# Optimization experiments

Measured on AMD Instinct MI355X. Metric: run time of the kernel, lower is better.

Reference implementation:

```python
import jax, jax.numpy as jnp
import numpy as np

B, L, E, H = 4, 2048, 512, 8
HD = E // H
EPS = 1e-6


def setup_inputs() -> dict:
    key = jax.random.key(0)
    ks = jax.random.split(key, 9)
    s = 0.02
    return {
        "query": jax.random.normal(ks[0], (B, L, E), dtype=jnp.float32),
        "Wq": jax.random.normal(ks[1], (E, E), dtype=jnp.float32) * s,
        "bq": jnp.zeros((E,), dtype=jnp.float32),
        "Wk": jax.random.normal(ks[2], (E, E), dtype=jnp.float32) * s,
        "bk": jnp.zeros((E,), dtype=jnp.float32),
        "Wv": jax.random.normal(ks[3], (E, E), dtype=jnp.float32) * s,
        "bv": jnp.zeros((E,), dtype=jnp.float32),
        "Wo": jax.random.normal(ks[4], (E, E), dtype=jnp.float32) * s,
        "bo": jnp.zeros((E,), dtype=jnp.float32),
    }


def reference(query, Wq, bq, Wk, bk, Wv, bv, Wo, bo):
    b, tgt_len, embed_dim = query.shape
    n_head = H
    head_dim = embed_dim // n_head
    # Faithful to the source: a raw view (reshape), NOT a transpose.
    x = query.reshape(tgt_len, b, embed_dim)  # (L, B, E)
    q = x @ Wq.T + bq
    k = x @ Wk.T + bk
    v = x @ Wv.T + bv
    # softmax over head_dim, per head
    q = jax.nn.softmax(q.reshape(tgt_len, b, n_head, head_dim), axis=-1)
    k = jax.nn.softmax(k.reshape(tgt_len, b, n_head, head_dim), axis=-1)
    # (L, B*H, hd) -> (B*H, L, hd)
    q_ = q.reshape(tgt_len, b * n_head, head_dim).swapaxes(0, 1)
    k_ = k.reshape(tgt_len, b * n_head, head_dim).swapaxes(0, 1)
    comp_q_ = 1.0 - q_
    comp_k_ = 1.0 - k_
    v_ = v.reshape(tgt_len, b * n_head, head_dim).swapaxes(0, 1)
    # non-causal XNor attention: scores from q.k^T + (1-q).(1-k)^T
    weights = jnp.einsum('nld,nsd->nls', q_, k_) + jnp.einsum('nld,nsd->nls', comp_q_, comp_k_)
    denom = jnp.clip(jnp.sum(weights, axis=-1, keepdims=True), EPS, None)
    attn_weights = weights / denom
    attn_output = jnp.einsum('nls,nsd->nld', attn_weights, v_)  # (B*H, L, hd)
    attn_output = attn_output.swapaxes(0, 1).reshape(tgt_len, b, embed_dim)
    out = attn_output @ Wo.T + bo
    return out.reshape(b, tgt_len, embed_dim)
```

## Files before the change

kernel.cpp:

```cpp
#include <hip/hip_runtime.h>

#define B_ 4
#define L_ 2048
#define E_ 512
#define H_ 8
#define NROW (B_*L_)
#define SZ (NROW*E_)
#define NH (B_*H_)

typedef unsigned short u16;
typedef unsigned int u32;
typedef __attribute__((ext_vector_type(8))) __bf16 bf16x8;
typedef __attribute__((ext_vector_type(8))) u16 u16x8;
typedef __attribute__((ext_vector_type(4))) float f32x4;

__device__ __forceinline__ u16 f2bf(float f) {
  union { float f; u32 u; } v; v.f = f;
  u32 r = v.u + 0x7FFFu + ((v.u >> 16) & 1u);
  return (u16)(r >> 16);
}
__device__ __forceinline__ float bf2f(u16 s) {
  union { u32 u; float f; } v; v.u = ((u32)s) << 16;
  return v.f;
}
__device__ __forceinline__ void async16(const u16* g, u16* l) {
  __builtin_amdgcn_global_load_lds(
      (const __attribute__((address_space(1))) u32*)g,
      (__attribute__((address_space(3))) u32*)l, 16, 0, 0);
}

__global__ __launch_bounds__(256) void cvt_all(const float* __restrict__ X,
    const float* __restrict__ W0, const float* __restrict__ W1,
    const float* __restrict__ W2, const float* __restrict__ W3,
    u16* __restrict__ Y, u16* __restrict__ Y0, u16* __restrict__ Y1,
    u16* __restrict__ Y2, u16* __restrict__ Y3) {
  const int bid = blockIdx.x;
  const float* src;
  u16* dst;
  int off;
  if (bid < 2048) { src = X; dst = Y; off = bid * 2048; }
  else {
    const int t = bid - 2048, s = t >> 7, r = t & 127;
    src = (s == 0) ? W0 : (s == 1) ? W1 : (s == 2) ? W2 : W3;
    dst = (s == 0) ? Y0 : (s == 1) ? Y1 : (s == 2) ? Y2 : Y3;
    off = r * 2048;
  }
  const int i0 = off + threadIdx.x * 8;
  f32x4 a = *(const f32x4*)(src + i0);
  f32x4 b = *(const f32x4*)(src + i0 + 4);
  u16x8 o;
#pragma unroll
  for (int j = 0; j < 4; ++j) { o[j] = f2bf(a[j]); o[4 + j] = f2bf(b[j]); }
  *(u16x8*)(dst + i0) = o;
}

__global__ __launch_bounds__(256) void qkv_gemm(const u16* __restrict__ X,
    const u16* __restrict__ Wq, const u16* __restrict__ Wk, const u16* __restrict__ Wv,
    const float* __restrict__ bq, const float* __restrict__ bk, const float* __restrict__ bv,
    u16* __restrict__ Qo, u16* __restrict__ Ko, u16* __restrict__ Vo) {
  __shared__ __align__(16) union {
    struct { u16 a[2][128 * 32]; u16 b[2][64 * 32]; } st;
    u16 ep[4][16 * 72];
  } sh;
  const int z = blockIdx.z;
  const u16* W = (z == 0) ? Wq : (z == 1) ? Wk : Wv;
  const float* bias = (z == 0) ? bq : (z == 1) ? bk : bv;
  u16* C = (z == 0) ? Qo : (z == 1) ? Ko : Vo;
  const int tid = threadIdx.x;
  const int w = tid >> 6, lane = tid & 63;
  const int bm = blockIdx.x * 128, bn = blockIdx.y * 64;
  const int fr = lane & 15, quad = lane >> 4;
  const int c0 = tid, c1 = tid + 256;
  const int ar0 = c0 >> 2, ak0 = (c0 & 3) * 8;
  const int ar1 = c1 >> 2, ak1 = (c1 & 3) * 8;
  f32x4 acc[2][4] = {};
  for (int k0 = 0; k0 < E_; k0 += 64) {
    __syncthreads();
#pragma unroll
    for (int p = 0; p < 2; ++p) {
      const int kp = k0 + p * 32;
      async16(X + (size_t)(bm + ar0) * E_ + kp + ak0, sh.st.a[p] + c0 * 8);
      async16(X + (size_t)(bm + ar1) * E_ + kp + ak1, sh.st.a[p] + c1 * 8);
      async16(W + (size_t)(bn + ar0) * E_ + kp + ak0, sh.st.b[p] + c0 * 8);
    }
    __syncthreads();
#pragma unroll
    for (int p = 0; p < 2; ++p) {
      bf16x8 af[2], bf[4];
#pragma unroll
      for (int mt = 0; mt < 2; ++mt)
        af[mt] = *(const bf16x8*)(sh.st.a[p] + (w * 32 + mt * 16 + fr) * 32 + quad * 8);
#pragma unroll
      for (int nt = 0; nt < 4; ++nt)
        bf[nt] = *(const bf16x8*)(sh.st.b[p] + (nt * 16 + fr) * 32 + quad * 8);
#pragma unroll
      for (int mt = 0; mt < 2; ++mt)
#pragma unroll
        for (int nt = 0; nt < 4; ++nt)
          acc[mt][nt] = __builtin_amdgcn_mfma_f32_16x16x32_bf16(af[mt], bf[nt],
                                                                acc[mt][nt], 0, 0, 0);
    }
  }
  __syncthreads();
  u16* ep = sh.ep[w];
#pragma unroll
  for (int mt = 0; mt < 2; ++mt) {
    if (z < 2) {
#pragma unroll
      for (int r = 0; r < 4; ++r) {
        float v[4];
#pragma unroll
        for (int nt = 0; nt < 4; ++nt)
          v[nt] = acc[mt][nt][r] + bias[bn + nt * 16 + fr];
        float mx = fmaxf(fmaxf(v[0], v[1]), fmaxf(v[2], v[3]));
#pragma unroll
        for (int off = 1; off < 16; off <<= 1) mx = fmaxf(mx, __shfl_xor(mx, off, 64));
        float e[4], ssum = 0.f;
#pragma unroll
        for (int nt = 0; nt < 4; ++nt) { e[nt] = __expf(v[nt] - mx); ssum += e[nt]; }
#pragma unroll
        for (int off = 1; off < 16; off <<= 1) ssum += __shfl_xor(ssum, off, 64);
        const float inv = 1.f / ssum;
#pragma unroll
        for (int nt = 0; nt < 4; ++nt)
          ep[(quad * 4 + r) * 72 + nt * 16 + fr] = f2bf(e[nt] * inv);
      }
    } else {
#pragma unroll
      for (int r = 0; r < 4; ++r)
#pragma unroll
        for (int nt = 0; nt < 4; ++nt)
          ep[(quad * 4 + r) * 72 + nt * 16 + fr] = f2bf(acc[mt][nt][r] + bias[bn + nt * 16 + fr]);
    }
#pragma unroll
    for (int pass = 0; pass < 2; ++pass) {
      const int row = pass * 8 + (lane >> 3), ch = lane & 7;
      u16x8 val = *(const u16x8*)(ep + row * 72 + ch * 8);
      *(u16x8*)(C + (size_t)(bm + w * 32 + mt * 16 + row) * E_ + bn + ch * 8) = val;
    }
  }
}

__global__ __launch_bounds__(256) void gemm_out(const u16* __restrict__ X,
    const u16* __restrict__ W, const float* __restrict__ bias, float* __restrict__ C) {
  __shared__ __align__(16) union {
    struct { u16 a[2][128 * 32]; u16 b[2][64 * 32]; } st;
    float ep[4][16 * 68];
  } sh;
  const int tid = threadIdx.x;
  const int w = tid >> 6, lane = tid & 63;
  const int bm = blockIdx.x * 128, bn = blockIdx.y * 64;
  const int fr = lane & 15, quad = lane >> 4;
  const int c0 = tid, c1 = tid + 256;
  const int ar0 = c0 >> 2, ak0 = (c0 & 3) * 8;
  const int ar1 = c1 >> 2, ak1 = (c1 & 3) * 8;
  f32x4 acc[2][4] = {};
  for (int k0 = 0; k0 < E_; k0 += 64) {
    __syncthreads();
#pragma unroll
    for (int p = 0; p < 2; ++p) {
      const int kp = k0 + p * 32;
      async16(X + (size_t)(bm + ar0) * E_ + kp + ak0, sh.st.a[p] + c0 * 8);
      async16(X + (size_t)(bm + ar1) * E_ + kp + ak1, sh.st.a[p] + c1 * 8);
      async16(W + (size_t)(bn + ar0) * E_ + kp + ak0, sh.st.b[p] + c0 * 8);
    }
    __syncthreads();
#pragma unroll
    for (int p = 0; p < 2; ++p) {
      bf16x8 af[2], bf[4];
#pragma unroll
      for (int mt = 0; mt < 2; ++mt)
        af[mt] = *(const bf16x8*)(sh.st.a[p] + (w * 32 + mt * 16 + fr) * 32 + quad * 8);
#pragma unroll
      for (int nt = 0; nt < 4; ++nt)
        bf[nt] = *(const bf16x8*)(sh.st.b[p] + (nt * 16 + fr) * 32 + quad * 8);
#pragma unroll
      for (int mt = 0; mt < 2; ++mt)
#pragma unroll
        for (int nt = 0; nt < 4; ++nt)
          acc[mt][nt] = __builtin_amdgcn_mfma_f32_16x16x32_bf16(af[mt], bf[nt],
                                                                acc[mt][nt], 0, 0, 0);
    }
  }
  __syncthreads();
  float* ep = sh.ep[w];
#pragma unroll
  for (int mt = 0; mt < 2; ++mt) {
#pragma unroll
    for (int r = 0; r < 4; ++r)
#pragma unroll
      for (int nt = 0; nt < 4; ++nt)
        ep[(quad * 4 + r) * 68 + nt * 16 + fr] = acc[mt][nt][r] + bias[bn + nt * 16 + fr];
#pragma unroll
    for (int p = 0; p < 4; ++p) {
      const int id = p * 64 + lane;
      const int row = id >> 4, ch = id & 15;
      f32x4 val = *(const f32x4*)(ep + row * 68 + ch * 4);
      *(f32x4*)(C + (size_t)(bm + w * 32 + mt * 16 + row) * E_ + bn + ch * 4) = val;
    }
  }
}

__global__ __launch_bounds__(256) void kv_part(const u16* __restrict__ K,
    const u16* __restrict__ V, float* __restrict__ Part,
    float* __restrict__ KPart, float* __restrict__ VPart) {
  const int n = blockIdx.x, b = n >> 3, h = n & 7;
  const int sy = blockIdx.y;
  const int tid = threadIdx.x;
  const int td = tid & 15, te = tid >> 4;
  __shared__ float sK[32][68], sV[32][68];
  float acc[4][4] = {};
  float srow = 0.f;
  const int which = tid >> 7, sub = tid & 127;
  const int lr = sub >> 2, ck = (sub & 3) * 16;
  const u16* src = which ? V : K;
  float* dstrow = which ? &sV[lr][ck] : &sK[lr][ck];
  const int l0beg = sy * 128;
  for (int l0 = l0beg; l0 < l0beg + 128; l0 += 32) {
    const u16* g = src + (size_t)((l0 + lr) * B_ + b) * E_ + h * 64 + ck;
    u16x8 d0 = *(const u16x8*)g;
    u16x8 d1 = *(const u16x8*)(g + 8);
    __syncthreads();
    f32x4 f0, f1, f2, f3;
#pragma unroll
    for (int j = 0; j < 4; ++j) {
      f0[j] = bf2f(d0[j]); f1[j] = bf2f(d0[4 + j]);
      f2[j] = bf2f(d1[j]); f3[j] = bf2f(d1[4 + j]);
    }
    *(f32x4*)(dstrow) = f0; *(f32x4*)(dstrow + 4) = f1;
    *(f32x4*)(dstrow + 8) = f2; *(f32x4*)(dstrow + 12) = f3;
    __syncthreads();
#pragma unroll 8
    for (int p = 0; p < 32; ++p) {
      f32x4 kk = *(const f32x4*)&sK[p][td * 4];
      f32x4 vv = *(const f32x4*)&sV[p][te * 4];
#pragma unroll
      for (int i = 0; i < 4; ++i)
#pragma unroll
        for (int j = 0; j < 4; ++j)
          acc[i][j] = fmaf(kk[i], vv[j], acc[i][j]);
      if (tid < 64) srow += sK[p][tid];
      else if (tid < 128) srow += sV[p][tid - 64];
    }
  }
  float* Pp = Part + (size_t)(n * 16 + sy) * 4096;
#pragma unroll
  for (int j = 0; j < 4; ++j) {
    f32x4 v4 = {acc[0][j], acc[1][j], acc[2][j], acc[3][j]};
    *(f32x4*)(Pp + (te * 4 + j) * 64 + td * 4) = v4;
  }
  if (tid < 64) KPart[(n * 16 + sy) * 64 + tid] = srow;
  else if (tid < 128) VPart[(n * 16 + sy) * 64 + tid - 64] = srow;
}

__global__ __launch_bounds__(256) void kv_merge(const float* __restrict__ Part,
    const float* __restrict__ KPart, const float* __restrict__ VPart,
    float* __restrict__ Mt, float* __restrict__ Ks, float* __restrict__ Vs) {
  const int bid = blockIdx.x, tid = threadIdx.x;
  if (bid < 512) {
    const int oi = bid * 256 + tid;
    const int n = oi >> 12, j = oi & 4095;
    const float* p = Part + (size_t)n * 16 * 4096 + j;
    float s = 0.f;
#pragma unroll
    for (int sl = 0; sl < 16; ++sl) s += p[sl * 4096];
    Mt[oi] = s;
  } else {
    const int i = (bid - 512) * 256 + tid;
    const int which = i >> 11, rem = i & 2047;
    const int n = rem >> 6, d = rem & 63;
    const float* p = (which ? VPart : KPart) + (n * 16) * 64 + d;
    float s = 0.f;
#pragma unroll
    for (int sl = 0; sl < 16; ++sl) s += p[sl * 64];
    if (which) Vs[n * 64 + d] = s; else Ks[n * 64 + d] = s;
  }
}

__global__ __launch_bounds__(256) void apply_mfma(const u16* __restrict__ Qbf,
    const float* __restrict__ Mt, const float* __restrict__ Ksum,
    const float* __restrict__ Vsum, u16* __restrict__ Abf) {
  __shared__ __align__(16) u16 sQ[128 * 64];
  __shared__ __align__(16) u16 sM[64 * 64];
  __shared__ float sKs[64], sVs[64], sDen[128];
  const int n = blockIdx.x, b = n >> 3, h = n & 7;
  const int l0 = blockIdx.y * 128;
  const int tid = threadIdx.x, w = tid >> 6, lane = tid & 63;
  const int fr = lane & 15, quad = lane >> 4;
#pragma unroll
  for (int j = 0; j < 4; ++j) {
    const int rloc = w * 32 + j * 8;
    const int row = rloc + (lane >> 3);
    const int k = (lane & 7) * 8;
    async16(Qbf + (size_t)((l0 + row) * B_ + b) * E_ + h * 64 + k, sQ + rloc * 64);
  }
  {
    const float* Mp = Mt + (size_t)n * 4096 + tid * 16;
    f32x4 m0 = *(const f32x4*)(Mp);
    f32x4 m1 = *(const f32x4*)(Mp + 4);
    f32x4 m2 = *(const f32x4*)(Mp + 8);
    f32x4 m3 = *(const f32x4*)(Mp + 12);
    u16x8 o0, o1;
#pragma unroll
    for (int j = 0; j < 4; ++j) {
      o0[j] = f2bf(m0[j]); o0[4 + j] = f2bf(m1[j]);
      o1[j] = f2bf(m2[j]); o1[4 + j] = f2bf(m3[j]);
    }
    *(u16x8*)(sM + tid * 16) = o0;
    *(u16x8*)(sM + tid * 16 + 8) = o1;
  }
  if (tid < 64) sKs[tid] = Ksum[n * 64 + tid];
  else if (tid < 128) sVs[tid - 64] = Vsum[n * 64 + tid - 64];
  __syncthreads();
  union { u16x8 u; bf16x8 bv; } aU[2][2];
  bf16x8 bF[4][2];
#pragma unroll
  for (int mt = 0; mt < 2; ++mt)
#pragma unroll
    for (int ks = 0; ks < 2; ++ks)
      aU[mt][ks].u = *(const u16x8*)(sQ + (w * 32 + mt * 16 + fr) * 64 + ks * 32 + quad * 8);
#pragma unroll
  for (int nt = 0; nt < 4; ++nt)
#pragma unroll
    for (int ks = 0; ks < 2; ++ks)
      bF[nt][ks] = *(const bf16x8*)(sM + (nt * 16 + fr) * 64 + ks * 32 + quad * 8);
  float pden[2] = {0.f, 0.f};
#pragma unroll
  for (int mt = 0; mt < 2; ++mt)
#pragma unroll
    for (int ks = 0; ks < 2; ++ks)
#pragma unroll
      for (int j = 0; j < 8; ++j)
        pden[mt] = fmaf(bf2f(aU[mt][ks].u[j]), sKs[ks * 32 + quad * 8 + j], pden[mt]);
#pragma unroll
  for (int mt = 0; mt < 2; ++mt) {
    pden[mt] += __shfl_xor(pden[mt], 16, 64);
    pden[mt] += __shfl_xor(pden[mt], 32, 64);
    if (quad == 0)
      sDen[w * 32 + mt * 16 + fr] = fmaxf(2.f * pden[mt] + 62.f * (float)L_, 1e-6f);
  }
  __syncthreads();
  f32x4 acc[2][4];
#pragma unroll
  for (int mt = 0; mt < 2; ++mt)
#pragma unroll
    for (int nt = 0; nt < 4; ++nt) {
      const float iv = 31.f * sVs[nt * 16 + fr];
      acc[mt][nt] = (f32x4){iv, iv, iv, iv};
#pragma unroll
      for (int ks = 0; ks < 2; ++ks)
        acc[mt][nt] = __builtin_amdgcn_mfma_f32_16x16x32_bf16(aU[mt][ks].bv, bF[nt][ks],
                                                              acc[mt][nt], 0, 0, 0);
    }
#pragma unroll
  for (int mt = 0; mt < 2; ++mt)
#pragma unroll
    for (int r = 0; r < 4; ++r) {
      const int rloc = w * 32 + mt * 16 + quad * 4 + r;
      const float invd = 2.f / sDen[rloc];
      const size_t orow = (size_t)((l0 + rloc) * B_ + b) * E_ + h * 64;
#pragma unroll
      for (int nt = 0; nt < 4; ++nt)
        Abf[orow + nt * 16 + fr] = f2bf(acc[mt][nt][r] * invd);
    }
}

extern "C" void kernel_launch(void* const* d_in, const int* in_sizes, int n_in,
                              void* d_out, int out_size, void* d_ws, size_t ws_size,
                              hipStream_t stream) {
  const float* query = (const float*)d_in[0];
  const float* Wq = (const float*)d_in[1];
  const float* bq = (const float*)d_in[2];
  const float* Wk = (const float*)d_in[3];
  const float* bk = (const float*)d_in[4];
  const float* Wv = (const float*)d_in[5];
  const float* bv = (const float*)d_in[6];
  const float* Wo = (const float*)d_in[7];
  const float* bo = (const float*)d_in[8];
  float* out = (float*)d_out;

  char* ws = (char*)d_ws;
  u16* Xbf  = (u16*)(ws);
  u16* Qbf  = (u16*)(ws + 8388608);
  u16* Kbf  = (u16*)(ws + 16777216);
  u16* Vbf  = (u16*)(ws + 25165824);
  u16* Abf  = (u16*)(ws + 33554432);
  u16* Wqb  = (u16*)(ws + 41943040);
  u16* Wkb  = (u16*)(ws + 42467328);
  u16* Wvb  = (u16*)(ws + 42991616);
  u16* Wob  = (u16*)(ws + 43515904);
  float* Mt = (float*)(ws + 44040192);
  float* Ks = (float*)(ws + 44564480);
  float* Vs = (float*)(ws + 44572672);
  float* KPart = (float*)(ws + 44580864);
  float* VPart = (float*)(ws + 44711936);
  float* Part  = (float*)Xbf;

  cvt_all<<<2560, 256, 0, stream>>>(query, Wq, Wk, Wv, Wo,
                                    Xbf, Wqb, Wkb, Wvb, Wob);
  qkv_gemm<<<dim3(NROW / 128, E_ / 64, 3), 256, 0, stream>>>(
      Xbf, Wqb, Wkb, Wvb, bq, bk, bv, Qbf, Kbf, Vbf);
  kv_part<<<dim3(NH, 16), 256, 0, stream>>>(Kbf, Vbf, Part, KPart, VPart);
  kv_merge<<<528, 256, 0, stream>>>(Part, KPart, VPart, Mt, Ks, Vs);
  apply_mfma<<<dim3(NH, L_ / 128), 256, 0, stream>>>(Qbf, Mt, Ks, Vs, Abf);
  gemm_out<<<dim3(NROW / 128, E_ / 64), 256, 0, stream>>>(Abf, Wob, bo, out);
}
```

Measured before the change: 145.6 us.

## Widen QKV GEMM tile to 128x128 and store merged KV state as bf16

The QKV projection GEMM now uses 128x128 output tiles, with each of the four waves computing a 64x64 sub-tile (4x4 MFMA tiles). This raises arithmetic intensity and halves the number of blocks, at the cost of more accumulator registers; an occupancy hint of three blocks per CU is added. Separately, kv_merge now writes the reduced KV matrix directly as bf16, and apply_mfma loads it with async copies instead of reading fp32 and converting per block. That halves the traffic for that matrix and removes redundant conversions.

```diff
diff --git a/kernel.cpp b/kernel.cpp
--- a/kernel.cpp
+++ b/kernel.cpp
@@ -54,12 +54,12 @@
   *(u16x8*)(dst + i0) = o;
 }
 
-__global__ __launch_bounds__(256) void qkv_gemm(const u16* __restrict__ X,
+__global__ __launch_bounds__(256, 3) void qkv_gemm(const u16* __restrict__ X,
     const u16* __restrict__ Wq, const u16* __restrict__ Wk, const u16* __restrict__ Wv,
     const float* __restrict__ bq, const float* __restrict__ bk, const float* __restrict__ bv,
     u16* __restrict__ Qo, u16* __restrict__ Ko, u16* __restrict__ Vo) {
   __shared__ __align__(16) union {
-    struct { u16 a[2][128 * 32]; u16 b[2][64 * 32]; } st;
+    struct { u16 a[2][128 * 32]; u16 b[2][128 * 32]; } st;
     u16 ep[4][16 * 72];
   } sh;
   const int z = blockIdx.z;
@@ -68,12 +68,13 @@
   u16* C = (z == 0) ? Qo : (z == 1) ? Ko : Vo;
   const int tid = threadIdx.x;
   const int w = tid >> 6, lane = tid & 63;
-  const int bm = blockIdx.x * 128, bn = blockIdx.y * 64;
+  const int bm = blockIdx.x * 128, bn = blockIdx.y * 128;
+  const int wm = (w >> 1) * 64, wn = (w & 1) * 64;
   const int fr = lane & 15, quad = lane >> 4;
   const int c0 = tid, c1 = tid + 256;
   const int ar0 = c0 >> 2, ak0 = (c0 & 3) * 8;
   const int ar1 = c1 >> 2, ak1 = (c1 & 3) * 8;
-  f32x4 acc[2][4] = {};
+  f32x4 acc[4][4] = {};
   for (int k0 = 0; k0 < E_; k0 += 64) {
     __syncthreads();
 #pragma unroll
@@ -82,36 +83,35 @@
       async16(X + (size_t)(bm + ar0) * E_ + kp + ak0, sh.st.a[p] + c0 * 8);
       async16(X + (size_t)(bm + ar1) * E_ + kp + ak1, sh.st.a[p] + c1 * 8);
       async16(W + (size_t)(bn + ar0) * E_ + kp + ak0, sh.st.b[p] + c0 * 8);
+      async16(W + (size_t)(bn + ar1) * E_ + kp + ak1, sh.st.b[p] + c1 * 8);
     }
     __syncthreads();
 #pragma unroll
     for (int p = 0; p < 2; ++p) {
-      bf16x8 af[2], bf[4];
-#pragma unroll
-      for (int mt = 0; mt < 2; ++mt)
-        af[mt] = *(const bf16x8*)(sh.st.a[p] + (w * 32 + mt * 16 + fr) * 32 + quad * 8);
-#pragma unroll
-      for (int nt = 0; nt < 4; ++nt)
-        bf[nt] = *(const bf16x8*)(sh.st.b[p] + (nt * 16 + fr) * 32 + quad * 8);
-#pragma unroll
-      for (int mt = 0; mt < 2; ++mt)
-#pragma unroll
-        for (int nt = 0; nt < 4; ++nt)
-          acc[mt][nt] = __builtin_amdgcn_mfma_f32_16x16x32_bf16(af[mt], bf[nt],
-                                                                acc[mt][nt], 0, 0, 0);
+      bf16x8 af[4], bf[4];
+#pragma unroll
+      for (int t = 0; t < 4; ++t) {
+        af[t] = *(const bf16x8*)(sh.st.a[p] + (wm + t * 16 + fr) * 32 + quad * 8);
+        bf[t] = *(const bf16x8*)(sh.st.b[p] + (wn + t * 16 + fr) * 32 + quad * 8);
+      }
+#pragma unroll
+      for (int i = 0; i < 4; ++i)
+#pragma unroll
+        for (int j = 0; j < 4; ++j)
+          acc[i][j] = __builtin_amdgcn_mfma_f32_16x16x32_bf16(af[i], bf[j], acc[i][j], 0, 0, 0);
     }
   }
   __syncthreads();
   u16* ep = sh.ep[w];
 #pragma unroll
-  for (int mt = 0; mt < 2; ++mt) {
+  for (int i = 0; i < 4; ++i) {
     if (z < 2) {
 #pragma unroll
       for (int r = 0; r < 4; ++r) {
         float v[4];
 #pragma unroll
         for (int nt = 0; nt < 4; ++nt)
-          v[nt] = acc[mt][nt][r] + bias[bn + nt * 16 + fr];
+          v[nt] = acc[i][nt][r] + bias[bn + wn + nt * 16 + fr];
         float mx = fmaxf(fmaxf(v[0], v[1]), fmaxf(v[2], v[3]));
 #pragma unroll
         for (int off = 1; off < 16; off <<= 1) mx = fmaxf(mx, __shfl_xor(mx, off, 64));
@@ -130,13 +130,14 @@
       for (int r = 0; r < 4; ++r)
 #pragma unroll
         for (int nt = 0; nt < 4; ++nt)
-          ep[(quad * 4 + r) * 72 + nt * 16 + fr] = f2bf(acc[mt][nt][r] + bias[bn + nt * 16 + fr]);
+          ep[(quad * 4 + r) * 72 + nt * 16 + fr] =
+              f2bf(acc[i][nt][r] + bias[bn + wn + nt * 16 + fr]);
     }
 #pragma unroll
     for (int pass = 0; pass < 2; ++pass) {
       const int row = pass * 8 + (lane >> 3), ch = lane & 7;
       u16x8 val = *(const u16x8*)(ep + row * 72 + ch * 8);
-      *(u16x8*)(C + (size_t)(bm + w * 32 + mt * 16 + row) * E_ + bn + ch * 8) = val;
+      *(u16x8*)(C + (size_t)(bm + wm + i * 16 + row) * E_ + bn + wn + ch * 8) = val;
     }
   }
 }
@@ -255,7 +256,7 @@
 
 __global__ __launch_bounds__(256) void kv_merge(const float* __restrict__ Part,
     const float* __restrict__ KPart, const float* __restrict__ VPart,
-    float* __restrict__ Mt, float* __restrict__ Ks, float* __restrict__ Vs) {
+    u16* __restrict__ Mtbf, float* __restrict__ Ks, float* __restrict__ Vs) {
   const int bid = blockIdx.x, tid = threadIdx.x;
   if (bid < 512) {
     const int oi = bid * 256 + tid;
@@ -264,7 +265,7 @@
     float s = 0.f;
 #pragma unroll
     for (int sl = 0; sl < 16; ++sl) s += p[sl * 4096];
-    Mt[oi] = s;
+    Mtbf[oi] = f2bf(s);
   } else {
     const int i = (bid - 512) * 256 + tid;
     const int which = i >> 11, rem = i & 2047;
@@ -278,7 +279,7 @@
 }
 
 __global__ __launch_bounds__(256) void apply_mfma(const u16* __restrict__ Qbf,
-    const float* __restrict__ Mt, const float* __restrict__ Ksum,
+    const u16* __restrict__ Mtbf, const float* __restrict__ Ksum,
     const float* __restrict__ Vsum, u16* __restrict__ Abf) {
   __shared__ __align__(16) u16 sQ[128 * 64];
   __shared__ __align__(16) u16 sM[64 * 64];
@@ -294,20 +295,10 @@
     const int k = (lane & 7) * 8;
     async16(Qbf + (size_t)((l0 + row) * B_ + b) * E_ + h * 64 + k, sQ + rloc * 64);
   }
-  {
-    const float* Mp = Mt + (size_t)n * 4096 + tid * 16;
-    f32x4 m0 = *(const f32x4*)(Mp);
-    f32x4 m1 = *(const f32x4*)(Mp + 4);
-    f32x4 m2 = *(const f32x4*)(Mp + 8);
-    f32x4 m3 = *(const f32x4*)(Mp + 12);
-    u16x8 o0, o1;
-#pragma unroll
-    for (int j = 0; j < 4; ++j) {
-      o0[j] = f2bf(m0[j]); o0[4 + j] = f2bf(m1[j]);
-      o1[j] = f2bf(m2[j]); o1[4 + j] = f2bf(m3[j]);
-    }
-    *(u16x8*)(sM + tid * 16) = o0;
-    *(u16x8*)(sM + tid * 16 + 8) = o1;
+#pragma unroll
+  for (int j = 0; j < 2; ++j) {
+    const int c = j * 256 + tid;
+    async16(Mtbf + (size_t)n * 4096 + c * 8, sM + c * 8);
   }
   if (tid < 64) sKs[tid] = Ksum[n * 64 + tid];
   else if (tid < 128) sVs[tid - 64] = Vsum[n * 64 + tid - 64];
@@ -389,7 +380,7 @@
   u16* Wkb  = (u16*)(ws + 42467328);
   u16* Wvb  = (u16*)(ws + 42991616);
   u16* Wob  = (u16*)(ws + 43515904);
-  float* Mt = (float*)(ws + 44040192);
+  u16* Mtbf = (u16*)(ws + 44040192);
   float* Ks = (float*)(ws + 44564480);
   float* Vs = (float*)(ws + 44572672);
   float* KPart = (float*)(ws + 44580864);
@@ -398,10 +389,10 @@
 
   cvt_all<<<2560, 256, 0, stream>>>(query, Wq, Wk, Wv, Wo,
                                     Xbf, Wqb, Wkb, Wvb, Wob);
-  qkv_gemm<<<dim3(NROW / 128, E_ / 64, 3), 256, 0, stream>>>(
+  qkv_gemm<<<dim3(NROW / 128, E_ / 128, 3), 256, 0, stream>>>(
       Xbf, Wqb, Wkb, Wvb, bq, bk, bv, Qbf, Kbf, Vbf);
   kv_part<<<dim3(NH, 16), 256, 0, stream>>>(Kbf, Vbf, Part, KPart, VPart);
-  kv_merge<<<528, 256, 0, stream>>>(Part, KPart, VPart, Mt, Ks, Vs);
-  apply_mfma<<<dim3(NH, L_ / 128), 256, 0, stream>>>(Qbf, Mt, Ks, Vs, Abf);
+  kv_merge<<<528, 256, 0, stream>>>(Part, KPart, VPart, Mtbf, Ks, Vs);
+  apply_mfma<<<dim3(NH, L_ / 128), 256, 0, stream>>>(Qbf, Mtbf, Ks, Vs, Abf);
   gemm_out<<<dim3(NROW / 128, E_ / 64), 256, 0, stream>>>(Abf, Wob, bo, out);
 }
```

Result: faster. 142.0 us (-2.5%).
